# Performance work log

Measured on AMD Instinct MI355X. Metric: run time of the kernel, lower is better.

The kernel has to match this reference:

```python
import jax, jax.numpy as jnp
import numpy as np

L, E, H, D = 28, 1024, 8, 128
THETA = 1000000.0
EPS = 1e-6
IMG_ENC_MAGNITUDE = 31.73
LAYER_INPUT_MAGNITUDES = [0.8584, 8.875, 12.2422, 703.5, 706.0, 707.5, 710.5, 712.0, 715.5, 718.0, 721.5, 728.0, 735.5, 739.0, 740.5, 740.5, 748.5, 763.5, 780.0, 800.0, 827.0, 860.0, 904.5, 952.5, 1003.0, 1071.0, 1146.0, 1174.0]


def setup_inputs() -> dict:
    key = jax.random.key(0)
    ks = jax.random.split(key, 5)
    B, S = 2, 1024
    image_context = jax.random.normal(ks[0], (B, S, E), dtype=jnp.float32)
    layer_scales = jnp.asarray(np.array(LAYER_INPUT_MAGNITUDES, dtype=np.float32) / IMG_ENC_MAGNITUDE)
    ln_w = 1.0 + 0.02 * jax.random.normal(ks[1], (L, E), dtype=jnp.float32)
    Wk = 0.02 * jax.random.normal(ks[2], (L, E, E), dtype=jnp.float32)
    Wv = 0.02 * jax.random.normal(ks[3], (L, E, E), dtype=jnp.float32)
    kn_w = 1.0 + 0.02 * jax.random.normal(ks[4], (L, D), dtype=jnp.float32)
    return {"image_context": image_context, "layer_scales": layer_scales,
            "ln_w": ln_w, "Wk": Wk, "Wv": Wv, "kn_w": kn_w}


def _rms_norm(x, w):
    # Qwen3 RMSNorm: x * rsqrt(mean(x^2) + eps) * weight
    return x * jax.lax.rsqrt(jnp.mean(x * x, axis=-1, keepdims=True) + EPS) * w


def _rotate_half(x):
    x1, x2 = x[..., : D // 2], x[..., D // 2 :]
    return jnp.concatenate([-x2, x1], axis=-1)


def _rope_cos_sin(S):
    inv_freq = 1.0 / (THETA ** (jnp.arange(0, D, 2, dtype=jnp.float32) / D))  # [D/2]
    freqs = jnp.arange(S, dtype=jnp.float32)[:, None] * inv_freq[None, :]     # [S, D/2]
    emb = jnp.concatenate([freqs, freqs], axis=-1)                            # [S, D]
    return jnp.cos(emb), jnp.sin(emb)


def reference(image_context, layer_scales, ln_w, Wk, Wv, kn_w):
    B, S, _ = image_context.shape
    cos, sin = _rope_cos_sin(S)  # [S, D] each

    # Per-layer scale + input RMSNorm, vectorized over layers -> [L, B, S, E]
    scaled = image_context[None] * layer_scales[:, None, None, None]
    normed = _rms_norm(scaled, ln_w[:, None, None, :])

    # K/V projections per layer: [L, B, S, E] x [L, E(out), E(in)] -> [L, B, S, E]
    k = jnp.einsum('lbse,lke->lbsk', normed, Wk).reshape(L, B, S, H, D)
    v = jnp.einsum('lbse,lke->lbsk', normed, Wv).reshape(L, B, S, H, D)

    # k_norm over head_dim, then move heads: [L, B, H, S, D]
    k = _rms_norm(k, kn_w[:, None, None, None, :]).transpose(0, 1, 3, 2, 4)
    v = v.transpose(0, 1, 3, 2, 4)

    # RoPE on keys (cos/sin broadcast over L, B, H)
    k_rot = k * cos + _rotate_half(k) * sin

    # Stacked KV cache: [2, L, B, H, S, D]
    return jnp.stack([k_rot, v])
```

## Files before the change

kernel.cpp:

```cpp
#include <hip/hip_runtime.h>

#define L_ 28
#define E_ 1024
#define H_ 8
#define D_ 128
#define B_ 2
#define S_ 1024

typedef __bf16 bf16x8 __attribute__((ext_vector_type(8)));
typedef float f32x4 __attribute__((ext_vector_type(4)));

__device__ __forceinline__ unsigned int f2bf2(float a, float b) {
  unsigned int ua = __builtin_bit_cast(unsigned int, a);
  ua += 0x7fffu + ((ua >> 16) & 1u);
  unsigned int ub = __builtin_bit_cast(unsigned int, b);
  ub += 0x7fffu + ((ub >> 16) & 1u);
  return (ua >> 16) | (ub & 0xffff0000u);
}

__device__ __forceinline__ void gll16(const void* g, void* l) {
  __builtin_amdgcn_global_load_lds(
      (const __attribute__((address_space(1))) unsigned int*)g,
      (__attribute__((address_space(3))) unsigned int*)l, 16, 0, 0);
}

#define TILE_B 16384
#define WS_W_OFF   0ull
#define WS_A_OFF   117440512ull
#define WS_SUM_OFF 121634816ull
#define WS_NEED    121643008ull

__global__ __launch_bounds__(256) void prep_w_kernel(
    const float* __restrict__ Wk, const float* __restrict__ Wv,
    const float* __restrict__ lnw, unsigned short* __restrict__ wsW)
{
  const int idx = blockIdx.x * 256 + threadIdx.x;
  const int tile = idx >> 10;
  const int p = idx & 1023;
  const int row = p >> 3;
  const int c = (p & 7) ^ (row & 7);
  const int ks = tile & 15;
  const int nb = (tile >> 4) & 7;
  const int kv = (tile >> 7) & 1;
  const int l  = tile >> 8;
  const float* src = (kv ? Wv : Wk) + (size_t)l * E_ * E_ +
                     (size_t)(nb * 128 + row) * E_ + ks * 64 + c * 8;
  const float* lw = lnw + l * E_ + ks * 64 + c * 8;
  const float4 w0 = *reinterpret_cast<const float4*>(src);
  const float4 w1 = *reinterpret_cast<const float4*>(src + 4);
  const float4 l0 = *reinterpret_cast<const float4*>(lw);
  const float4 l1 = *reinterpret_cast<const float4*>(lw + 4);
  uint4 o;
  o.x = f2bf2(w0.x * l0.x, w0.y * l0.y);
  o.y = f2bf2(w0.z * l0.z, w0.w * l0.w);
  o.z = f2bf2(w1.x * l1.x, w1.y * l1.y);
  o.w = f2bf2(w1.z * l1.z, w1.w * l1.w);
  *reinterpret_cast<uint4*>(reinterpret_cast<char*>(wsW) + (size_t)idx * 16) = o;
}

__global__ __launch_bounds__(256) void prep_x_kernel(
    const float* __restrict__ x, unsigned short* __restrict__ wsA,
    float* __restrict__ wsSum)
{
  const int lane = threadIdx.x & 63;
  const int r = blockIdx.x * 4 + (threadIdx.x >> 6);
  const int mb = r >> 7, rt = r & 127;
  const float* src = x + (size_t)r * E_;
  float sq = 0.f;
  #pragma unroll
  for (int it = 0; it < 2; ++it) {
    const int j = it * 64 + lane;
    const int ksj = j >> 3, cj = j & 7;
    const float4 a0 = *reinterpret_cast<const float4*>(src + j * 8);
    const float4 a1 = *reinterpret_cast<const float4*>(src + j * 8 + 4);
    sq += a0.x * a0.x + a0.y * a0.y + a0.z * a0.z + a0.w * a0.w +
          a1.x * a1.x + a1.y * a1.y + a1.z * a1.z + a1.w * a1.w;
    uint4 o;
    o.x = f2bf2(a0.x, a0.y);
    o.y = f2bf2(a0.z, a0.w);
    o.z = f2bf2(a1.x, a1.y);
    o.w = f2bf2(a1.z, a1.w);
    const size_t pos = (size_t)(mb * 16 + ksj) * 1024 + rt * 8 + (cj ^ (rt & 7));
    *reinterpret_cast<uint4*>(reinterpret_cast<char*>(wsA) + pos * 16) = o;
  }
  #pragma unroll
  for (int off = 1; off < 64; off <<= 1) sq += __shfl_xor(sq, off, 64);
  if (lane == 0) wsSum[r] = sq;
}

__global__ __launch_bounds__(256, 2) void fused_main_kernel(
    const unsigned short* __restrict__ wsA,
    const unsigned short* __restrict__ wsW,
    const float* __restrict__ wsSum,
    const float* __restrict__ scales,
    const float* __restrict__ knw,
    float* __restrict__ out)
{
  __shared__ unsigned short sA[8192];
  __shared__ unsigned short sK[8192];
  __shared__ unsigned short sV[8192];
  __shared__ float s_sumsq[128];
  __shared__ float s_knw[128];

  const int t = threadIdx.x;
  const int logical = (blockIdx.x & 7) * 448 + (blockIdx.x >> 3);
  const int l = logical >> 7;
  const int n_idx = (logical >> 4) & 7;
  const int m_idx = logical & 15;

  if (t < 128) {
    s_sumsq[t] = wsSum[m_idx * 128 + t];
    s_knw[t] = knw[l * D_ + t];
  }

  const int lane = t & 63;
  const int wv = t >> 6;
  const int col16 = lane & 15;
  const int quad = lane >> 4;

  const char* gA = reinterpret_cast<const char*>(wsA) + (size_t)(m_idx * 16) * TILE_B;
  const char* gK = reinterpret_cast<const char*>(wsW) + (size_t)((l * 2 + 0) * 8 + n_idx) * 16 * TILE_B;
  const char* gV = reinterpret_cast<const char*>(wsW) + (size_t)((l * 2 + 1) * 8 + n_idx) * 16 * TILE_B;
  const int lnoff = wv * 4096 + lane * 16;

  const int slot0 = ((quad)     ^ (col16 & 7)) << 4;
  const int slot1 = ((quad + 4) ^ (col16 & 7)) << 4;
  const int arow = (wv * 32 + col16) * 128;
  const int brow = col16 * 128;
  const char* pA = reinterpret_cast<const char*>(sA);
  const char* pK = reinterpret_cast<const char*>(sK);
  const char* pV = reinterpret_cast<const char*>(sV);

  f32x4 accK[2][8], accV[2][8];
  #pragma unroll
  for (int i = 0; i < 2; ++i)
    #pragma unroll
    for (int j = 0; j < 8; ++j) {
      accK[i][j] = (f32x4){0.f, 0.f, 0.f, 0.f};
      accV[i][j] = (f32x4){0.f, 0.f, 0.f, 0.f};
    }

  for (int ks = 0; ks < 16; ++ks) {
    __syncthreads();
    const char* a = gA + (size_t)ks * TILE_B;
    const char* k = gK + (size_t)ks * TILE_B;
    const char* v = gV + (size_t)ks * TILE_B;
    #pragma unroll
    for (int j = 0; j < 4; ++j) {
      const int so = wv * 4096 + j * 1024;
      gll16(a + lnoff + j * 1024, (char*)sA + so);
      gll16(k + lnoff + j * 1024, (char*)sK + so);
      gll16(v + lnoff + j * 1024, (char*)sV + so);
    }
    __syncthreads();

    #pragma unroll
    for (int kk = 0; kk < 2; ++kk) {
      const int sl = kk ? slot1 : slot0;
      bf16x8 a0 = *reinterpret_cast<const bf16x8*>(pA + arow + sl);
      bf16x8 a1 = *reinterpret_cast<const bf16x8*>(pA + arow + 2048 + sl);
      #pragma unroll
      for (int nt = 0; nt < 8; ++nt) {
        bf16x8 bk = *reinterpret_cast<const bf16x8*>(pK + brow + nt * 2048 + sl);
        accK[0][nt] = __builtin_amdgcn_mfma_f32_16x16x32_bf16(a0, bk, accK[0][nt], 0, 0, 0);
        accK[1][nt] = __builtin_amdgcn_mfma_f32_16x16x32_bf16(a1, bk, accK[1][nt], 0, 0, 0);
        bf16x8 bv = *reinterpret_cast<const bf16x8*>(pV + brow + nt * 2048 + sl);
        accV[0][nt] = __builtin_amdgcn_mfma_f32_16x16x32_bf16(a0, bv, accV[0][nt], 0, 0, 0);
        accV[1][nt] = __builtin_amdgcn_mfma_f32_16x16x32_bf16(a1, bv, accV[1][nt], 0, 0, 0);
      }
    }
  }

  const int m_base = m_idx * 128;
  const float scale = scales[l];
  float freq[8], kw8[8];
  #pragma unroll
  for (int nt = 0; nt < 8; ++nt) {
    const int d = nt * 16 + col16;
    freq[nt] = exp2f(-(float)(d & 63) * 0.31143075889569023f);
    kw8[nt] = s_knw[d];
  }
  const size_t VOFF = (size_t)L_ * B_ * H_ * S_ * D_;

  #pragma unroll
  for (int mt = 0; mt < 2; ++mt) {
    #pragma unroll
    for (int reg = 0; reg < 4; ++reg) {
      const int rl = wv * 32 + mt * 16 + quad * 4 + reg;
      const int mg = m_base + rl;
      const int bb = mg >> 10;
      const int ss = mg & 1023;
      const float ms = s_sumsq[rl] * (1.0f / 1024.0f);
      const float rho = scale * rsqrtf(scale * scale * ms + 1e-6f);
      float kvv[8], vvv[8];
      float ksum = 0.f;
      #pragma unroll
      for (int nt = 0; nt < 8; ++nt) {
        kvv[nt] = rho * accK[mt][nt][reg];
        vvv[nt] = rho * accV[mt][nt][reg];
        ksum += kvv[nt] * kvv[nt];
      }
      #pragma unroll
      for (int off = 1; off < 16; off <<= 1) ksum += __shfl_xor(ksum, off, 64);
      const float r2 = rsqrtf(ksum * (1.0f / 128.0f) + 1e-6f);
      float kn[8];
      #pragma unroll
      for (int nt = 0; nt < 8; ++nt) kn[nt] = kvv[nt] * r2 * kw8[nt];
      const float sf = (float)ss;
      const size_t base = ((((size_t)(l * B_ + bb)) * H_ + n_idx) * S_ + ss) * D_;
      #pragma unroll
      for (int nt = 0; nt < 8; ++nt) {
        const float ang = sf * freq[nt];
        const float cs = __cosf(ang);
        const float sn = __sinf(ang);
        const float rot = (nt < 4) ? -kn[nt + 4] : kn[nt - 4];
        out[base + nt * 16 + col16] = kn[nt] * cs + rot * sn;
        out[VOFF + base + nt * 16 + col16] = vvv[nt];
      }
    }
  }
}

__global__ __launch_bounds__(256, 2) void fused_kv_kernel(
    const float* __restrict__ x, const float* __restrict__ scales,
    const float* __restrict__ lnw, const float* __restrict__ Wk,
    const float* __restrict__ Wv, const float* __restrict__ knw,
    float* __restrict__ out)
{
  __shared__ unsigned short sA[128][72];
  __shared__ unsigned short sK[128][72];
  __shared__ unsigned short sV[128][72];
  __shared__ float s_lnw[E_];
  __shared__ float s_knw[D_];
  __shared__ float s_sumsq[128];

  const int t = threadIdx.x;
  const int bx = blockIdx.x;
  const int l = bx >> 7;
  const int n_idx = (bx >> 4) & 7;
  const int m_idx = bx & 15;
  const int m_base = m_idx * 128;
  const int n_base = n_idx * 128;

  *reinterpret_cast<float4*>(&s_lnw[t * 4]) =
      *reinterpret_cast<const float4*>(&lnw[(size_t)l * E_ + t * 4]);
  if (t < D_) s_knw[t] = knw[l * D_ + t];

  const int c4 = t & 15;
  const int r0 = t >> 4;

  const float* xg  = x  + (size_t)(m_base + r0) * E_ + c4 * 4;
  const float* wkg = Wk + (size_t)l * E_ * E_ + (size_t)(n_base + r0) * E_ + c4 * 4;
  const float* wvg = Wv + (size_t)l * E_ * E_ + (size_t)(n_base + r0) * E_ + c4 * 4;

  const int lane = t & 63;
  const int wv = t >> 6;
  const int col16 = lane & 15;
  const int quad = lane >> 4;

  f32x4 accK[2][8], accV[2][8];
  #pragma unroll
  for (int i = 0; i < 2; ++i)
    #pragma unroll
    for (int j = 0; j < 8; ++j) {
      accK[i][j] = (f32x4){0.f, 0.f, 0.f, 0.f};
      accV[i][j] = (f32x4){0.f, 0.f, 0.f, 0.f};
    }
  float sq[8] = {0.f, 0.f, 0.f, 0.f, 0.f, 0.f, 0.f, 0.f};

  for (int ks = 0; ks < 16; ++ks) {
    const int k0 = ks * 64;
    float4 av[8];
    #pragma unroll
    for (int p = 0; p < 8; ++p)
      av[p] = *reinterpret_cast<const float4*>(xg + (size_t)(p * 16) * E_ + k0);

    __syncthreads();

    #pragma unroll
    for (int p = 0; p < 8; ++p) {
      sq[p] += av[p].x * av[p].x + av[p].y * av[p].y +
               av[p].z * av[p].z + av[p].w * av[p].w;
      uint2 pk;
      pk.x = f2bf2(av[p].x, av[p].y);
      pk.y = f2bf2(av[p].z, av[p].w);
      *reinterpret_cast<uint2*>(&sA[r0 + p * 16][c4 * 4]) = pk;
    }
    const float4 lw = *reinterpret_cast<const float4*>(&s_lnw[k0 + c4 * 4]);
    #pragma unroll
    for (int p = 0; p < 8; ++p) {
      float4 w4 = *reinterpret_cast<const float4*>(wkg + (size_t)(p * 16) * E_ + k0);
      uint2 pk;
      pk.x = f2bf2(w4.x * lw.x, w4.y * lw.y);
      pk.y = f2bf2(w4.z * lw.z, w4.w * lw.w);
      *reinterpret_cast<uint2*>(&sK[r0 + p * 16][c4 * 4]) = pk;
    }
    #pragma unroll
    for (int p = 0; p < 8; ++p) {
      float4 w4 = *reinterpret_cast<const float4*>(wvg + (size_t)(p * 16) * E_ + k0);
      uint2 pk;
      pk.x = f2bf2(w4.x * lw.x, w4.y * lw.y);
      pk.y = f2bf2(w4.z * lw.z, w4.w * lw.w);
      *reinterpret_cast<uint2*>(&sV[r0 + p * 16][c4 * 4]) = pk;
    }
    __syncthreads();

    #pragma unroll
    for (int kk = 0; kk < 2; ++kk) {
      const int ko = kk * 32 + quad * 8;
      bf16x8 a0 = *reinterpret_cast<const bf16x8*>(&sA[wv * 32 + col16][ko]);
      bf16x8 a1 = *reinterpret_cast<const bf16x8*>(&sA[wv * 32 + 16 + col16][ko]);
      #pragma unroll
      for (int nt = 0; nt < 8; ++nt) {
        bf16x8 bk = *reinterpret_cast<const bf16x8*>(&sK[nt * 16 + col16][ko]);
        accK[0][nt] = __builtin_amdgcn_mfma_f32_16x16x32_bf16(a0, bk, accK[0][nt], 0, 0, 0);
        accK[1][nt] = __builtin_amdgcn_mfma_f32_16x16x32_bf16(a1, bk, accK[1][nt], 0, 0, 0);
        bf16x8 bv = *reinterpret_cast<const bf16x8*>(&sV[nt * 16 + col16][ko]);
        accV[0][nt] = __builtin_amdgcn_mfma_f32_16x16x32_bf16(a0, bv, accV[0][nt], 0, 0, 0);
        accV[1][nt] = __builtin_amdgcn_mfma_f32_16x16x32_bf16(a1, bv, accV[1][nt], 0, 0, 0);
      }
    }
  }

  __syncthreads();
  float* red = reinterpret_cast<float*>(&sA[0][0]);
  #pragma unroll
  for (int p = 0; p < 8; ++p) red[(r0 + p * 16) * 16 + c4] = sq[p];
  __syncthreads();
  if (t < 128) {
    float s = 0.f;
    #pragma unroll
    for (int i = 0; i < 16; ++i) s += red[t * 16 + i];
    s_sumsq[t] = s;
  }
  __syncthreads();

  const float scale = scales[l];
  float freq[8], kw8[8];
  #pragma unroll
  for (int nt = 0; nt < 8; ++nt) {
    const int d = nt * 16 + col16;
    freq[nt] = exp2f(-(float)(d & 63) * 0.31143075889569023f);
    kw8[nt] = s_knw[d];
  }
  const size_t VOFF = (size_t)L_ * B_ * H_ * S_ * D_;

  #pragma unroll
  for (int mt = 0; mt < 2; ++mt) {
    #pragma unroll
    for (int reg = 0; reg < 4; ++reg) {
      const int rl = wv * 32 + mt * 16 + quad * 4 + reg;
      const int mg = m_base + rl;
      const int bb = mg >> 10;
      const int ss = mg & 1023;
      const float ms = s_sumsq[rl] * (1.0f / 1024.0f);
      const float rho = scale * rsqrtf(scale * scale * ms + 1e-6f);
      float kvv[8], vvv[8];
      float ksum = 0.f;
      #pragma unroll
      for (int nt = 0; nt < 8; ++nt) {
        kvv[nt] = rho * accK[mt][nt][reg];
        vvv[nt] = rho * accV[mt][nt][reg];
        ksum += kvv[nt] * kvv[nt];
      }
      #pragma unroll
      for (int off = 1; off < 16; off <<= 1) ksum += __shfl_xor(ksum, off, 64);
      const float r2 = rsqrtf(ksum * (1.0f / 128.0f) + 1e-6f);
      float kn[8];
      #pragma unroll
      for (int nt = 0; nt < 8; ++nt) kn[nt] = kvv[nt] * r2 * kw8[nt];
      const float sf = (float)ss;
      const size_t base = ((((size_t)(l * B_ + bb)) * H_ + n_idx) * S_ + ss) * D_;
      #pragma unroll
      for (int nt = 0; nt < 8; ++nt) {
        const float ang = sf * freq[nt];
        const float cs = __cosf(ang);
        const float sn = __sinf(ang);
        const float rot = (nt < 4) ? -kn[nt + 4] : kn[nt - 4];
        out[base + nt * 16 + col16] = kn[nt] * cs + rot * sn;
        out[VOFF + base + nt * 16 + col16] = vvv[nt];
      }
    }
  }
}

extern "C" void kernel_launch(void* const* d_in, const int* in_sizes, int n_in,
                              void* d_out, int out_size, void* d_ws, size_t ws_size,
                              hipStream_t stream) {
  const float* x      = (const float*)d_in[0];
  const float* scales = (const float*)d_in[1];
  const float* lnw    = (const float*)d_in[2];
  const float* Wk     = (const float*)d_in[3];
  const float* Wv     = (const float*)d_in[4];
  const float* knw    = (const float*)d_in[5];
  float* out = (float*)d_out;

  if (d_ws != nullptr && ws_size >= WS_NEED) {
    unsigned short* wsW = (unsigned short*)((char*)d_ws + WS_W_OFF);
    unsigned short* wsA = (unsigned short*)((char*)d_ws + WS_A_OFF);
    float* wsSum        = (float*)((char*)d_ws + WS_SUM_OFF);
    prep_w_kernel<<<dim3(28672), 256, 0, stream>>>(Wk, Wv, lnw, wsW);
    prep_x_kernel<<<dim3(512), 256, 0, stream>>>(x, wsA, wsSum);
    fused_main_kernel<<<dim3(L_ * 16 * 8), 256, 0, stream>>>(wsA, wsW, wsSum, scales, knw, out);
  } else {
    fused_kv_kernel<<<dim3(L_ * 16 * 8), 256, 0, stream>>>(x, scales, lnw, Wk, Wv, knw, out);
  }
}
```

Measured before the change: 849.7 us.

## Double-buffer K/V weight tiles and load activations directly into registers

Changes the activation workspace to a plain row-major bf16 layout and has each lane load its A fragments straight from global memory into registers, prefetching the next k-step. The K and V weight tiles are now double-buffered in LDS, so the loads for step ks+1 are issued before the MFMAs of step ks, with one barrier per iteration instead of two. The aim is to hide global load latency behind compute and cut LDS traffic for A. The cost is more register pressure from the prefetched A fragments and extra LDS for the second buffers, and the direct A loads may be less coalesced.

Result: slower. 970.4 us (+14.2%).

```diff
diff --git a/kernel.cpp b/kernel.cpp
--- a/kernel.cpp
+++ b/kernel.cpp
@@ -64,13 +64,12 @@
 {
   const int lane = threadIdx.x & 63;
   const int r = blockIdx.x * 4 + (threadIdx.x >> 6);
-  const int mb = r >> 7, rt = r & 127;
   const float* src = x + (size_t)r * E_;
+  unsigned short* dst = wsA + (size_t)r * E_;
   float sq = 0.f;
   #pragma unroll
   for (int it = 0; it < 2; ++it) {
     const int j = it * 64 + lane;
-    const int ksj = j >> 3, cj = j & 7;
     const float4 a0 = *reinterpret_cast<const float4*>(src + j * 8);
     const float4 a1 = *reinterpret_cast<const float4*>(src + j * 8 + 4);
     sq += a0.x * a0.x + a0.y * a0.y + a0.z * a0.z + a0.w * a0.w +
@@ -80,8 +79,7 @@
     o.y = f2bf2(a0.z, a0.w);
     o.z = f2bf2(a1.x, a1.y);
     o.w = f2bf2(a1.z, a1.w);
-    const size_t pos = (size_t)(mb * 16 + ksj) * 1024 + rt * 8 + (cj ^ (rt & 7));
-    *reinterpret_cast<uint4*>(reinterpret_cast<char*>(wsA) + pos * 16) = o;
+    *reinterpret_cast<uint4*>(dst + j * 8) = o;
   }
   #pragma unroll
   for (int off = 1; off < 64; off <<= 1) sq += __shfl_xor(sq, off, 64);
@@ -96,9 +94,8 @@
     const float* __restrict__ knw,
     float* __restrict__ out)
 {
-  __shared__ unsigned short sA[8192];
-  __shared__ unsigned short sK[8192];
-  __shared__ unsigned short sV[8192];
+  __shared__ unsigned short sK[2][8192];
+  __shared__ unsigned short sV[2][8192];
   __shared__ float s_sumsq[128];
   __shared__ float s_knw[128];
 
@@ -118,18 +115,15 @@
   const int col16 = lane & 15;
   const int quad = lane >> 4;
 
-  const char* gA = reinterpret_cast<const char*>(wsA) + (size_t)(m_idx * 16) * TILE_B;
   const char* gK = reinterpret_cast<const char*>(wsW) + (size_t)((l * 2 + 0) * 8 + n_idx) * 16 * TILE_B;
   const char* gV = reinterpret_cast<const char*>(wsW) + (size_t)((l * 2 + 1) * 8 + n_idx) * 16 * TILE_B;
   const int lnoff = wv * 4096 + lane * 16;
 
+  const unsigned short* aRow = wsA + (size_t)(m_idx * 128 + wv * 32 + col16) * E_ + quad * 8;
+
   const int slot0 = ((quad)     ^ (col16 & 7)) << 4;
   const int slot1 = ((quad + 4) ^ (col16 & 7)) << 4;
-  const int arow = (wv * 32 + col16) * 128;
   const int brow = col16 * 128;
-  const char* pA = reinterpret_cast<const char*>(sA);
-  const char* pK = reinterpret_cast<const char*>(sK);
-  const char* pV = reinterpret_cast<const char*>(sV);
 
   f32x4 accK[2][8], accV[2][8];
   #pragma unroll
@@ -140,25 +134,46 @@
       accV[i][j] = (f32x4){0.f, 0.f, 0.f, 0.f};
     }
 
+  #pragma unroll
+  for (int j = 0; j < 4; ++j) {
+    const int so = wv * 4096 + j * 1024;
+    gll16(gK + lnoff + j * 1024, (char*)sK[0] + so);
+    gll16(gV + lnoff + j * 1024, (char*)sV[0] + so);
+  }
+  bf16x8 aC00 = *reinterpret_cast<const bf16x8*>(aRow);
+  bf16x8 aC01 = *reinterpret_cast<const bf16x8*>(aRow + 32);
+  bf16x8 aC10 = *reinterpret_cast<const bf16x8*>(aRow + 16 * E_);
+  bf16x8 aC11 = *reinterpret_cast<const bf16x8*>(aRow + 16 * E_ + 32);
+  __syncthreads();
+
+  int cur = 0;
   for (int ks = 0; ks < 16; ++ks) {
-    __syncthreads();
-    const char* a = gA + (size_t)ks * TILE_B;
-    const char* k = gK + (size_t)ks * TILE_B;
-    const char* v = gV + (size_t)ks * TILE_B;
-    #pragma unroll
-    for (int j = 0; j < 4; ++j) {
-      const int so = wv * 4096 + j * 1024;
-      gll16(a + lnoff + j * 1024, (char*)sA + so);
-      gll16(k + lnoff + j * 1024, (char*)sK + so);
-      gll16(v + lnoff + j * 1024, (char*)sV + so);
-    }
-    __syncthreads();
-
+    if (ks < 15) {
+      const char* k = gK + (size_t)(ks + 1) * TILE_B;
+      const char* v = gV + (size_t)(ks + 1) * TILE_B;
+      char* dK = (char*)sK[cur ^ 1];
+      char* dV = (char*)sV[cur ^ 1];
+      #pragma unroll
+      for (int j = 0; j < 4; ++j) {
+        const int so = wv * 4096 + j * 1024;
+        gll16(k + lnoff + j * 1024, dK + so);
+        gll16(v + lnoff + j * 1024, dV + so);
+      }
+    }
+    const int ksn = (ks < 15) ? (ks + 1) : ks;
+    const unsigned short* an = aRow + ksn * 64;
+    bf16x8 aN00 = *reinterpret_cast<const bf16x8*>(an);
+    bf16x8 aN01 = *reinterpret_cast<const bf16x8*>(an + 32);
+    bf16x8 aN10 = *reinterpret_cast<const bf16x8*>(an + 16 * E_);
+    bf16x8 aN11 = *reinterpret_cast<const bf16x8*>(an + 16 * E_ + 32);
+
+    const char* pK = (const char*)sK[cur];
+    const char* pV = (const char*)sV[cur];
     #pragma unroll
     for (int kk = 0; kk < 2; ++kk) {
       const int sl = kk ? slot1 : slot0;
-      bf16x8 a0 = *reinterpret_cast<const bf16x8*>(pA + arow + sl);
-      bf16x8 a1 = *reinterpret_cast<const bf16x8*>(pA + arow + 2048 + sl);
+      const bf16x8 a0 = kk ? aC01 : aC00;
+      const bf16x8 a1 = kk ? aC11 : aC10;
       #pragma unroll
       for (int nt = 0; nt < 8; ++nt) {
         bf16x8 bk = *reinterpret_cast<const bf16x8*>(pK + brow + nt * 2048 + sl);
@@ -169,6 +184,9 @@
         accV[1][nt] = __builtin_amdgcn_mfma_f32_16x16x32_bf16(a1, bv, accV[1][nt], 0, 0, 0);
       }
     }
+    __syncthreads();
+    aC00 = aN00; aC01 = aN01; aC10 = aN10; aC11 = aN11;
+    cur ^= 1;
   }
 
   const int m_base = m_idx * 128;
```
